# Kernel tuning notes

Hardware: AMD Instinct MI355X
Metric: run time of the kernel (lower is better)

## Reference

```python
import jax, jax.numpy as jnp
import numpy as np

N, C, HW, HEADS = 2048, 16, 8, 4
F = C * HW * HW  # 1024
E = 16384
EPS = 1e-5
NEG_SLOPE = 0.2


def _bn(x, g, b):
    # training-mode BatchNorm2d over (N, H, W)
    m = x.mean(axis=(0, 2, 3), keepdims=True)
    v = x.var(axis=(0, 2, 3), keepdims=True)
    return (x - m) * jax.lax.rsqrt(v + EPS) * g[None, :, None, None] + b[None, :, None, None]


def _conv1x1(x, w, b):
    # 1x1 conv == per-pixel linear: w is [out_c, in_c]
    return jnp.einsum('nchw,oc->nohw', x, w) + b[None, :, None, None]


def _gatv2(xf, edge_index, wl, bl, wr, br, att, bias_gat):
    # xf: [N, F] node features
    xl = (xf @ wl + bl).reshape(N, HEADS, F)  # source-side transform (lin_l)
    xr = (xf @ wr + br).reshape(N, HEADS, F)  # target-side transform (lin_r)
    src, dst = edge_index[0], edge_index[1]
    loops = jnp.arange(N)
    # PyG default: remove existing self loops (mask them) then add self loops
    src_f = jnp.concatenate([src, loops])
    dst_f = jnp.concatenate([dst, loops])
    valid = jnp.concatenate([src != dst, jnp.ones((N,), bool)])
    xj = xl[src_f]                                   # [E+N, HEADS, F] gather
    e = jax.nn.leaky_relu(xj + xr[dst_f], negative_slope=NEG_SLOPE)
    logits = jnp.einsum('ehf,hf->eh', e, att)        # [E+N, HEADS]
    logits = jnp.where(valid[:, None], logits, -jnp.inf)
    mx = jax.lax.stop_gradient(jax.ops.segment_max(logits, dst_f, num_segments=N))
    expv = jnp.where(valid[:, None], jnp.exp(logits - mx[dst_f]), 0.0)
    denom = jax.ops.segment_sum(expv, dst_f, num_segments=N)
    alpha = expv / denom[dst_f]                      # segment softmax over incoming edges
    out = jax.ops.segment_sum(alpha[:, :, None] * xj, dst_f, num_segments=N)  # [N, HEADS, F]
    return out.reshape(N, HEADS * F) + bias_gat


def setup_inputs() -> dict:
    key = jax.random.key(0)
    ks = jax.random.split(key, 8)
    s = 0.02
    return {
        'x': jax.random.normal(ks[0], (N, C, HW, HW), jnp.float32),
        'edge_index': jax.random.randint(ks[1], (2, E), 0, N),
        'w1': jax.random.normal(ks[2], (C, C), jnp.float32) * s,
        'b1': jnp.zeros((C,), jnp.float32),
        'g1': jnp.ones((C,), jnp.float32),
        'be1': jnp.zeros((C,), jnp.float32),
        'wl': jax.random.normal(ks[3], (F, HEADS * F), jnp.float32) * s,
        'bl': jnp.zeros((HEADS * F,), jnp.float32),
        'wr': jax.random.normal(ks[4], (F, HEADS * F), jnp.float32) * s,
        'br': jnp.zeros((HEADS * F,), jnp.float32),
        'att': jax.random.normal(ks[5], (HEADS, F), jnp.float32) * s,
        'bias_gat': jnp.zeros((HEADS * F,), jnp.float32),
        'w2': jax.random.normal(ks[6], (C, HEADS * C), jnp.float32) * s,
        'b2': jnp.zeros((C,), jnp.float32),
        'g2': jnp.ones((C,), jnp.float32),
        'be2': jnp.zeros((C,), jnp.float32),
    }


def reference(x, edge_index, w1, b1, g1, be1, wl, bl, wr, br, att, bias_gat, w2, b2, g2, be2):
    res = x
    y = _bn(_conv1x1(x, w1, b1), g1, be1)            # fc1: Conv2d 1x1 + BN
    yf = y.reshape(N, F)
    g = _gatv2(yf, edge_index, wl, bl, wr, br, att, bias_gat)
    g = g.reshape(N, HEADS * C, HW, HW)
    out = _bn(_conv1x1(g, w2, b2), g2, be2)          # fc2: Conv2d 1x1 + BN
    return out + res                                  # DropPath(0.0) == Identity
```

## Files before the change

kernel.cpp:

```cpp
#include <hip/hip_runtime.h>
#include <stdint.h>

#define N_NODES 2048
#define F_DIM   1024
#define HEADS   4
#define NF      4096
#define ROW     8192
#define E_EDGES 16384
#define MAXE    (E_EDGES + N_NODES)
#define BN_EPS  1e-5f
#define NSLOPE  0.2f

typedef unsigned short ushort_t;
typedef __attribute__((ext_vector_type(8))) short bf16x8;
typedef __attribute__((ext_vector_type(4))) float f32x4;
typedef __attribute__((ext_vector_type(8))) unsigned short us8;

__device__ __forceinline__ float b2f(unsigned short u) {
    union { unsigned int i; float f; } x; x.i = ((unsigned int)u) << 16; return x.f;
}
__device__ __forceinline__ unsigned short f2b(float f) {
    union { float f; unsigned int i; } x; x.f = f;
    unsigned int r = x.i + 0x7fffu + ((x.i >> 16) & 1u);
    return (unsigned short)(r >> 16);
}
__device__ __forceinline__ ushort_t ld_canon(const void* src, size_t i, int f32) {
    return f32 ? f2b(((const float*)src)[i]) : ((const ushort_t*)src)[i];
}
__device__ __forceinline__ float ld_f(const void* src, size_t i, int f32) {
    return f32 ? ((const float*)src)[i] : b2f(((const ushort_t*)src)[i]);
}

__device__ __forceinline__ int sniff_f32_blk(const ushort_t* xu, int* lds_flag) {
    int t = threadIdx.x;
    if (t < 64) {
        unsigned e = (xu[2 * t] >> 7) & 0xFF;
        unsigned long long m = __ballot(e >= 0x90u);
        if (t == 0) *lds_flag = (__popcll(m) >= 3) ? 1 : 0;
    }
    __syncthreads();
    return *lds_flag;
}
__device__ __forceinline__ int sniff_i64_blk(const int* ei_raw, int* lds_flag) {
    int t = threadIdx.x;
    if (t < 64) {
        unsigned long long m = __ballot(ei_raw[2 * t + 1] != 0);
        if (t == 0) *lds_flag = (m == 0ull) ? 1 : 0;
    }
    __syncthreads();
    return *lds_flag;
}

__global__ __launch_bounds__(256) void k_prep(
    const void* __restrict__ wl, const void* __restrict__ wr,
    const int* __restrict__ ei_raw, const ushort_t* __restrict__ xu,
    const void* __restrict__ x, const void* __restrict__ w1, const void* __restrict__ b1,
    ushort_t* __restrict__ wT, int* __restrict__ counts,
    ushort_t* __restrict__ y0b, float* __restrict__ ps, float* __restrict__ pq)
{
    __shared__ ushort_t tl[64][65];
    __shared__ float xs[1024];
    __shared__ float sw[256];
    __shared__ float sb[16];
    __shared__ int sfl;
    int b = blockIdx.x, t = threadIdx.x;
    if (b < 2048) {
        int f32 = sniff_f32_blk(xu, &sfl);
        int z = b >> 10, rem = b & 1023;
        int bx = (rem & 63) * 64, by = (rem >> 6) * 64;
        const void* in = z ? wr : wl;
        ushort_t* outT = wT + (size_t)z * 4194304ull;
        #pragma unroll
        for (int i = 0; i < 16; ++i) {
            int idx = t + i * 256;
            int r = idx >> 6, c = idx & 63;
            tl[r][c] = ld_canon(in, (size_t)(by + r) * 4096 + bx + c, f32);
        }
        __syncthreads();
        #pragma unroll
        for (int i = 0; i < 16; ++i) {
            int idx = t + i * 256;
            int r = idx >> 6, c = idx & 63;
            outT[(size_t)(bx + r) * 1024 + by + c] = tl[c][r];
        }
    } else if (b < 2120) {
        int i64 = sniff_i64_blk(ei_raw, &sfl);
        int idx = (b - 2048) * 256 + t;
        if (idx < E_EDGES) {
            int s = i64 ? ei_raw[2 * idx] : ei_raw[idx];
            int d = i64 ? ei_raw[2 * (E_EDGES + idx)] : ei_raw[E_EDGES + idx];
            if (s != d) atomicAdd(&counts[d], 1);
        } else if (idx < MAXE) {
            atomicAdd(&counts[idx - E_EDGES], 1);
        }
    } else {
        int bid = b - 2120;
        int f32 = sniff_f32_blk(xu, &sfl);
        sw[t] = ld_f(w1, t, f32);
        if (t < 16) sb[t] = ld_f(b1, t, f32);
        int wave = t >> 6, lane = t & 63;
        float s[4] = {0,0,0,0}, q[4] = {0,0,0,0};
        for (int nn = 0; nn < 8; ++nn) {
            int n = bid * 8 + nn;
            __syncthreads();
            #pragma unroll
            for (int i = 0; i < 4; ++i) {
                int idx = t + i * 256;
                xs[idx] = ld_f(x, (size_t)n * 1024 + idx, f32);
            }
            __syncthreads();
            #pragma unroll
            for (int i = 0; i < 4; ++i) {
                int o = wave * 4 + i;
                float acc = sb[o];
                #pragma unroll
                for (int c = 0; c < 16; ++c) acc += xs[c * 64 + lane] * sw[o * 16 + c];
                y0b[(size_t)n * 1024 + o * 64 + lane] = f2b(acc);
                s[i] += acc; q[i] += acc * acc;
            }
        }
        #pragma unroll
        for (int i = 0; i < 4; ++i)
            for (int mm = 1; mm < 64; mm <<= 1) {
                s[i] += __shfl_xor(s[i], mm);
                q[i] += __shfl_xor(q[i], mm);
            }
        if (lane == 0)
            #pragma unroll
            for (int i = 0; i < 4; ++i) {
                ps[bid * 16 + wave * 4 + i] = s[i];
                pq[bid * 16 + wave * 4 + i] = q[i];
            }
    }
}

__global__ __launch_bounds__(256) void k_scatnorm(
    const int* __restrict__ ei_raw, const int* __restrict__ counts,
    int* __restrict__ cursor, int* __restrict__ offs, int* __restrict__ esrc,
    const ushort_t* __restrict__ y0b,
    const float* __restrict__ ps, const float* __restrict__ pq,
    const void* __restrict__ g1, const void* __restrict__ be1,
    const ushort_t* __restrict__ xu, ushort_t* __restrict__ xf)
{
    __shared__ int offl[2048];
    __shared__ int ts[256];
    __shared__ int sfl;
    __shared__ float red[2][64];
    __shared__ float scs[16], shs[16];
    int t = threadIdx.x;
    if (blockIdx.x < 72) {
        int i64 = sniff_i64_blk(ei_raw, &sfl);
        int loc[8]; int tot = 0;
        #pragma unroll
        for (int j = 0; j < 8; ++j) { loc[j] = counts[t * 8 + j]; tot += loc[j]; }
        ts[t] = tot; __syncthreads();
        for (int s = 1; s < 256; s <<= 1) {
            int v = (t >= s) ? ts[t - s] : 0;
            __syncthreads();
            ts[t] += v;
            __syncthreads();
        }
        int run = ts[t] - tot;
        #pragma unroll
        for (int j = 0; j < 8; ++j) { offl[t * 8 + j] = run; run += loc[j]; }
        __syncthreads();
        if (blockIdx.x == 0) {
            #pragma unroll
            for (int j = 0; j < 8; ++j) offs[t * 8 + j] = offl[t * 8 + j];
            if (t == 255) offs[2048] = run;
        }
        int idx = blockIdx.x * 256 + t;
        if (idx < E_EDGES) {
            int s = i64 ? ei_raw[2 * idx] : ei_raw[idx];
            int d = i64 ? ei_raw[2 * (E_EDGES + idx)] : ei_raw[E_EDGES + idx];
            if (s != d) esrc[offl[d] + atomicAdd(&cursor[d], 1)] = s;
        } else if (idx < MAXE) {
            int n = idx - E_EDGES;
            esrc[offl[n] + atomicAdd(&cursor[n], 1)] = n;
        }
    } else {
        int f32 = sniff_f32_blk(xu, &sfl);
        int lane = t & 63, wv = t >> 6;
        float s = 0.f, q = 0.f;
        #pragma unroll
        for (int i = 0; i < 16; ++i) { s += ps[i * 256 + t]; q += pq[i * 256 + t]; }
        s += __shfl_xor(s, 16); q += __shfl_xor(q, 16);
        s += __shfl_xor(s, 32); q += __shfl_xor(q, 32);
        if (lane < 16) { red[0][wv * 16 + lane] = s; red[1][wv * 16 + lane] = q; }
        __syncthreads();
        if (t < 16) {
            float S = red[0][t] + red[0][16 + t] + red[0][32 + t] + red[0][48 + t];
            float Q = red[1][t] + red[1][16 + t] + red[1][32 + t] + red[1][48 + t];
            const float inv = 1.0f / 131072.0f;
            float mean = S * inv;
            float var  = Q * inv - mean * mean;
            float sc = ld_f(g1, t, f32) * rsqrtf(var + BN_EPS);
            scs[t] = sc;
            shs[t] = ld_f(be1, t, f32) - mean * sc;
        }
        __syncthreads();
        size_t base = (size_t)(blockIdx.x - 72) * 4096 + t * 16;
        int ch = ((int)(base >> 6)) & 15;
        float sc = scs[ch], sh = shs[ch];
        us8 v0 = *(const us8*)(y0b + base), v1 = *(const us8*)(y0b + base + 8);
        us8 o0, o1;
        #pragma unroll
        for (int j = 0; j < 8; ++j) {
            o0[j] = f2b(b2f(v0[j]) * sc + sh);
            o1[j] = f2b(b2f(v1[j]) * sc + sh);
        }
        *(us8*)(xf + base) = o0;
        *(us8*)(xf + base + 8) = o1;
    }
}

__global__ __launch_bounds__(512) void k_gemm(
    const ushort_t* __restrict__ A, const ushort_t* __restrict__ BT,
    const void* __restrict__ blr, const void* __restrict__ brr,
    const ushort_t* __restrict__ xu, ushort_t* __restrict__ out)
{
    __shared__ __align__(16) ushort_t smem[65536];
    __shared__ int sfl;
    int f32 = sniff_f32_blk(xu, &sfl);
    int tid = threadIdx.x;
    int wv = tid >> 6, ln = tid & 63;
    int m0 = blockIdx.y * 256, n0 = blockIdx.x * 256;
    int wm = (wv >> 2) * 128, wn = (wv & 3) * 64;
    int lr = ln & 15, quad = ln >> 4;
    int key = (lr >> 1) & 3;

    f32x4 acc[8][4];
    #pragma unroll
    for (int i = 0; i < 8; ++i)
        #pragma unroll
        for (int j = 0; j < 4; ++j) acc[i][j] = (f32x4){0.f, 0.f, 0.f, 0.f};

    auto stage_panel = [&](const ushort_t* G, int row0, int kt, int slot, int which) {
        ushort_t* base = smem + which * 32768 + slot * 8192;
        #pragma unroll
        for (int j = 0; j < 2; ++j) {
            int c = wv * 128 + j * 64 + ln;
            int r = c >> 2;
            int q = (c & 3) ^ ((r >> 1) & 3);
            const ushort_t* g = G + (size_t)(row0 + r) * 1024 + kt * 32 + q * 8;
            __builtin_amdgcn_global_load_lds(
                (const __attribute__((address_space(1))) void*)g,
                (__attribute__((address_space(3))) void*)(base + (wv * 128 + j * 64) * 8),
                16, 0, 0);
        }
    };

    auto compute_tile = [&](int t) {
        const ushort_t* Ab = smem + (t & 3) * 8192;
        const ushort_t* Bb = smem + 32768 + (t & 3) * 8192;
        bf16x8 bfrag[4];
        #pragma unroll
        for (int j = 0; j < 4; ++j) {
            int col = wn + j * 16 + lr;
            bfrag[j] = *(const bf16x8*)(Bb + col * 32 + ((quad ^ key) * 8));
        }
        #pragma unroll
        for (int i = 0; i < 8; ++i) {
            int row = wm + i * 16 + lr;
            bf16x8 af = *(const bf16x8*)(Ab + row * 32 + ((quad ^ key) * 8));
            #pragma unroll
            for (int j = 0; j < 4; ++j)
                acc[i][j] = __builtin_amdgcn_mfma_f32_16x16x32_bf16(af, bfrag[j], acc[i][j], 0, 0, 0);
        }
    };

    stage_panel(A, m0, 0, 0, 0); stage_panel(BT, n0, 0, 0, 1);
    stage_panel(A, m0, 1, 1, 0); stage_panel(BT, n0, 1, 1, 1);
    stage_panel(A, m0, 2, 2, 0); stage_panel(BT, n0, 2, 2, 1);

    #pragma unroll 1
    for (int t = 0; t < 29; ++t) {
        asm volatile("s_waitcnt vmcnt(8)" ::: "memory");
        __builtin_amdgcn_s_barrier();
        int tn = t + 3;
        stage_panel(A, m0, tn, tn & 3, 0);
        stage_panel(BT, n0, tn, tn & 3, 1);
        compute_tile(t);
    }
    asm volatile("s_waitcnt vmcnt(8)" ::: "memory");
    __builtin_amdgcn_s_barrier();
    compute_tile(29);
    asm volatile("s_waitcnt vmcnt(4)" ::: "memory");
    __builtin_amdgcn_s_barrier();
    compute_tile(30);
    asm volatile("s_waitcnt vmcnt(0)" ::: "memory");
    __builtin_amdgcn_s_barrier();
    compute_tile(31);

    __syncthreads();
    float bj[4];
    #pragma unroll
    for (int j = 0; j < 4; ++j) {
        int colg = n0 + wn + j * 16 + lr;
        bj[j] = (colg < 4096) ? ld_f(blr, colg, f32) : ld_f(brr, colg - 4096, f32);
    }
    ushort_t* cs = smem;
    #pragma unroll
    for (int ph = 0; ph < 2; ++ph) {
        if ((wv >> 2) == ph) {
            #pragma unroll
            for (int i = 0; i < 8; ++i)
                #pragma unroll
                for (int j = 0; j < 4; ++j) {
                    int col = wn + j * 16 + lr;
                    #pragma unroll
                    for (int r = 0; r < 4; ++r)
                        cs[(i * 16 + quad * 4 + r) * 264 + col] = f2b(acc[i][j][r] + bj[j]);
                }
        }
        __syncthreads();
        #pragma unroll
        for (int rr = 0; rr < 8; ++rr) {
            int slot = rr * 512 + tid;
            int row = slot >> 5, seg = slot & 31;
            us8 v = *(const us8*)&cs[row * 264 + seg * 8];
            *(us8*)(out + (size_t)(m0 + ph * 128 + row) * ROW + n0 + seg * 8) = v;
        }
        __syncthreads();
    }
}

__global__ __launch_bounds__(64) void k_gat(
    const ushort_t* __restrict__ xlr,
    const void* __restrict__ att, const void* __restrict__ bg,
    const ushort_t* __restrict__ xu,
    const int* __restrict__ offsets, const int* __restrict__ esrc,
    ushort_t* __restrict__ g)
{
    int bx = blockIdx.x;
    int d = bx >> 2, h = bx & 3;
    int l = threadIdx.x;
    int f32;
    {
        unsigned e = (xu[2 * l] >> 7) & 0xFF;
        unsigned long long m = __ballot(e >= 0x90u);
        f32 = (__popcll(m) >= 3) ? 1 : 0;
    }
    int off = offsets[d], deg = offsets[d + 1] - off;
    size_t hF = (size_t)h * F_DIM + l * 16;

    float xrv[16], attv[16];
    {
        const ushort_t* xp = xlr + ((size_t)d * ROW + NF + hF);
        us8 x0 = *(const us8*)xp, x1 = *(const us8*)(xp + 8);
        #pragma unroll
        for (int j = 0; j < 8; ++j) {
            xrv[j] = b2f(x0[j]); xrv[8 + j] = b2f(x1[j]);
            attv[j]     = ld_f(att, hF + j, f32);
            attv[8 + j] = ld_f(att, hF + 8 + j, f32);
        }
    }
    float acc[16];
    #pragma unroll
    for (int j = 0; j < 16; ++j) acc[j] = 0.f;
    float s_run = 0.f;

    for (int c0 = 0; c0 < deg; c0 += 64) {
        int cnt = min(64, deg - c0);
        int eidx = esrc[off + c0 + (l < cnt ? l : 0)];
        int e = 0;
        for (; e + 3 < cnt; e += 4) {
            int i0 = __shfl(eidx, e),     i1 = __shfl(eidx, e + 1);
            int i2 = __shfl(eidx, e + 2), i3 = __shfl(eidx, e + 3);
            const ushort_t* p0 = xlr + ((size_t)i0 * ROW + hF);
            const ushort_t* p1 = xlr + ((size_t)i1 * ROW + hF);
            const ushort_t* p2 = xlr + ((size_t)i2 * ROW + hF);
            const ushort_t* p3 = xlr + ((size_t)i3 * ROW + hF);
            us8 v0[4], v1[4];
            v0[0] = *(const us8*)p0; v1[0] = *(const us8*)(p0 + 8);
            v0[1] = *(const us8*)p1; v1[1] = *(const us8*)(p1 + 8);
            v0[2] = *(const us8*)p2; v1[2] = *(const us8*)(p2 + 8);
            v0[3] = *(const us8*)p3; v1[3] = *(const us8*)(p3 + 8);
            float tt[4];
            #pragma unroll
            for (int k = 0; k < 4; ++k) {
                float t0 = 0.f;
                #pragma unroll
                for (int j = 0; j < 8; ++j) {
                    float u;
                    u = b2f(v0[k][j]) + xrv[j];     u = u > 0.f ? u : NSLOPE * u; t0 += u * attv[j];
                    u = b2f(v1[k][j]) + xrv[8 + j]; u = u > 0.f ? u : NSLOPE * u; t0 += u * attv[8 + j];
                }
                tt[k] = t0;
            }
            #pragma unroll
            for (int mm = 1; mm < 64; mm <<= 1) {
                tt[0] += __shfl_xor(tt[0], mm);
                tt[1] += __shfl_xor(tt[1], mm);
                tt[2] += __shfl_xor(tt[2], mm);
                tt[3] += __shfl_xor(tt[3], mm);
            }
            float w0 = __expf(tt[0]), w1 = __expf(tt[1]);
            float w2v = __expf(tt[2]), w3 = __expf(tt[3]);
            s_run += w0 + w1 + w2v + w3;
            #pragma unroll
            for (int j = 0; j < 8; ++j) {
                acc[j]     += w0 * b2f(v0[0][j]) + w1 * b2f(v0[1][j])
                            + w2v * b2f(v0[2][j]) + w3 * b2f(v0[3][j]);
                acc[8 + j] += w0 * b2f(v1[0][j]) + w1 * b2f(v1[1][j])
                            + w2v * b2f(v1[2][j]) + w3 * b2f(v1[3][j]);
            }
        }
        for (; e < cnt; ++e) {
            int i0 = __shfl(eidx, e);
            const ushort_t* p = xlr + ((size_t)i0 * ROW + hF);
            us8 a0 = *(const us8*)p, a1 = *(const us8*)(p + 8);
            float t0 = 0.f;
            #pragma unroll
            for (int j = 0; j < 8; ++j) {
                float u;
                u = b2f(a0[j]) + xrv[j];     u = u > 0.f ? u : NSLOPE * u; t0 += u * attv[j];
                u = b2f(a1[j]) + xrv[8 + j]; u = u > 0.f ? u : NSLOPE * u; t0 += u * attv[8 + j];
            }
            #pragma unroll
            for (int mm = 1; mm < 64; mm <<= 1) t0 += __shfl_xor(t0, mm);
            float w0 = __expf(t0);
            s_run += w0;
            #pragma unroll
            for (int j = 0; j < 8; ++j) {
                acc[j]     += w0 * b2f(a0[j]);
                acc[8 + j] += w0 * b2f(a1[j]);
            }
        }
    }
    float inv = 1.0f / s_run;
    ushort_t* gp = g + ((size_t)d * NF + hF);
    us8 outv0, outv1;
    #pragma unroll
    for (int j = 0; j < 8; ++j) {
        outv0[j] = f2b(acc[j] * inv + ld_f(bg, hF + j, f32));
        outv1[j] = f2b(acc[8 + j] * inv + ld_f(bg, hF + 8 + j, f32));
    }
    *(us8*)gp = outv0;
    *(us8*)(gp + 8) = outv1;
}

__global__ __launch_bounds__(256) void k_fc2(
    const ushort_t* __restrict__ g, const void* __restrict__ w2, const void* __restrict__ b2,
    const ushort_t* __restrict__ xu,
    ushort_t* __restrict__ zb, float* __restrict__ ps, float* __restrict__ pq)
{
    __shared__ float gs[4096];
    __shared__ float sw[1024];
    __shared__ float sb[16];
    __shared__ int sfl;
    int f32 = sniff_f32_blk(xu, &sfl);
    int tid = threadIdx.x;
    #pragma unroll
    for (int i = 0; i < 4; ++i) sw[tid + i * 256] = ld_f(w2, tid + i * 256, f32);
    if (tid < 16) sb[tid] = ld_f(b2, tid, f32);
    int wave = tid >> 6, lane = tid & 63;
    float s[4] = {0,0,0,0}, q[4] = {0,0,0,0};
    for (int nn = 0; nn < 2; ++nn) {
        int n = blockIdx.x * 2 + nn;
        __syncthreads();
        {
            const ushort_t* gp = g + (size_t)n * 4096 + tid * 16;
            us8 v0 = *(const us8*)gp, v1 = *(const us8*)(gp + 8);
            #pragma unroll
            for (int j = 0; j < 8; ++j) {
                gs[tid * 16 + j] = b2f(v0[j]);
                gs[tid * 16 + 8 + j] = b2f(v1[j]);
            }
        }
        __syncthreads();
        float acc[4];
        #pragma unroll
        for (int i = 0; i < 4; ++i) acc[i] = sb[wave * 4 + i];
        #pragma unroll 8
        for (int k = 0; k < 64; ++k) {
            float gv = gs[k * 64 + lane];
            #pragma unroll
            for (int i = 0; i < 4; ++i)
                acc[i] += gv * sw[(wave * 4 + i) * 64 + k];
        }
        #pragma unroll
        for (int i = 0; i < 4; ++i) {
            zb[(size_t)n * 1024 + (wave * 4 + i) * 64 + lane] = f2b(acc[i]);
            s[i] += acc[i]; q[i] += acc[i] * acc[i];
        }
    }
    #pragma unroll
    for (int i = 0; i < 4; ++i)
        for (int mm = 1; mm < 64; mm <<= 1) {
            s[i] += __shfl_xor(s[i], mm);
            q[i] += __shfl_xor(q[i], mm);
        }
    if (lane == 0)
        #pragma unroll
        for (int i = 0; i < 4; ++i) {
            ps[blockIdx.x * 16 + wave * 4 + i] = s[i];
            pq[blockIdx.x * 16 + wave * 4 + i] = q[i];
        }
}

__global__ __launch_bounds__(256) void k_out(
    const ushort_t* __restrict__ zb, const void* __restrict__ x,
    const float* __restrict__ ps, const float* __restrict__ pq,
    const void* __restrict__ g2, const void* __restrict__ be2,
    void* __restrict__ out)
{
    __shared__ float red[2][64];
    __shared__ float scs[16], shs[16];
    __shared__ int sfl;
    int f32 = sniff_f32_blk((const ushort_t*)x, &sfl);
    int t = threadIdx.x, lane = t & 63, wv = t >> 6;
    float s = 0.f, q = 0.f;
    #pragma unroll
    for (int i = 0; i < 64; ++i) { s += ps[i * 256 + t]; q += pq[i * 256 + t]; }
    s += __shfl_xor(s, 16); q += __shfl_xor(q, 16);
    s += __shfl_xor(s, 32); q += __shfl_xor(q, 32);
    if (lane < 16) { red[0][wv * 16 + lane] = s; red[1][wv * 16 + lane] = q; }
    __syncthreads();
    if (t < 16) {
        float S = red[0][t] + red[0][16 + t] + red[0][32 + t] + red[0][48 + t];
        float Q = red[1][t] + red[1][16 + t] + red[1][32 + t] + red[1][48 + t];
        const float inv = 1.0f / 131072.0f;
        float mean = S * inv;
        float var  = Q * inv - mean * mean;
        float sc = ld_f(g2, t, f32) * rsqrtf(var + BN_EPS);
        scs[t] = sc;
        shs[t] = ld_f(be2, t, f32) - mean * sc;
    }
    __syncthreads();
    size_t base = (size_t)blockIdx.x * 4096;
    #pragma unroll
    for (int i = 0; i < 16; ++i) {
        size_t k = base + t + i * 256;
        int ch = ((int)k >> 6) & 15;
        float val = b2f(zb[k]) * scs[ch] + shs[ch] + ld_f(x, k, f32);
        if (f32) ((float*)out)[k] = val;
        else     ((ushort_t*)out)[k] = f2b(val);
    }
}

extern "C" void kernel_launch(void* const* d_in, const int* in_sizes, int n_in,
                              void* d_out, int out_size, void* d_ws, size_t ws_size,
                              hipStream_t stream)
{
    const void* x   = d_in[0];
    const void* ei  = d_in[1];
    const void* w1  = d_in[2];
    const void* b1  = d_in[3];
    const void* g1  = d_in[4];
    const void* be1 = d_in[5];
    const void* wl  = d_in[6];
    const void* bl  = d_in[7];
    const void* wr  = d_in[8];
    const void* br  = d_in[9];
    const void* att = d_in[10];
    const void* bg  = d_in[11];
    const void* w2  = d_in[12];
    const void* b2  = d_in[13];
    const void* g2  = d_in[14];
    const void* be2 = d_in[15];
    (void)in_sizes; (void)n_in; (void)out_size; (void)ws_size;

    char* wsb = (char*)d_ws;
    size_t o = 0;
    auto alloc = [&](size_t bytes) -> void* {
        void* p = wsb + o;
        o = (o + bytes + 255) & ~(size_t)255;
        return p;
    };
    ushort_t* y0b   = (ushort_t*)alloc(2097152ull * 2);
    ushort_t* xf    = (ushort_t*)alloc(2097152ull * 2);
    ushort_t* zb    = (ushort_t*)alloc(2097152ull * 2);
    ushort_t* wT    = (ushort_t*)alloc(8388608ull * 2);
    ushort_t* gbuf  = wT;
    ushort_t* xlr   = (ushort_t*)alloc(16777216ull * 2);
    float* p1s = (float*)alloc(256 * 16 * 4);
    float* p1q = (float*)alloc(256 * 16 * 4);
    float* p2s = (float*)alloc(1024 * 16 * 4);
    float* p2q = (float*)alloc(1024 * 16 * 4);
    int* counts = (int*)alloc(2048 * 4);
    int* cursor = (int*)alloc(2048 * 4);
    int* offs   = (int*)alloc(2049 * 4);
    int* esrc   = (int*)alloc(MAXE * 4);

    hipMemsetAsync(counts, 0, 2 * 2048 * 4, stream);
    k_prep<<<2376, 256, 0, stream>>>(wl, wr, (const int*)ei, (const ushort_t*)x,
                                     x, w1, b1, wT, counts, y0b, p1s, p1q);
    k_scatnorm<<<584, 256, 0, stream>>>((const int*)ei, counts, cursor, offs, esrc,
                                        y0b, p1s, p1q, g1, be1, (const ushort_t*)x, xf);
    k_gemm<<<dim3(32, 8), 512, 0, stream>>>(xf, wT, bl, br, (const ushort_t*)x, xlr);
    k_gat<<<N_NODES * HEADS, 64, 0, stream>>>(xlr, att, bg, (const ushort_t*)x, offs, esrc, gbuf);
    k_fc2<<<1024, 256, 0, stream>>>(gbuf, w2, b2, (const ushort_t*)x, zb, p2s, p2q);
    k_out<<<512, 256, 0, stream>>>(zb, x, p2s, p2q, g2, be2, d_out);
}
```

Baseline: 261.7 us.

## Vectorize weight transpose and reshape GEMM pipeline to depth two with occupancy hint

The weight transpose in k_prep now loads and stores 8 bf16 values per access, with a padded LDS tile, instead of scalar element accesses. The GEMM prefetch depth drops from three tiles in flight to two, inside a single uniform loop with a sched_barrier. It also requests two blocks per CU through launch_bounds. Together these aim to cut transpose memory traffic and register pressure, trading some latency hiding for possible occupancy gains, though 128 KB of LDS per block may stop two blocks from fitting anyway.

```diff
diff --git a/kernel.cpp b/kernel.cpp
--- a/kernel.cpp
+++ b/kernel.cpp
@@ -58,7 +58,7 @@
     ushort_t* __restrict__ wT, int* __restrict__ counts,
     ushort_t* __restrict__ y0b, float* __restrict__ ps, float* __restrict__ pq)
 {
-    __shared__ ushort_t tl[64][65];
+    __shared__ ushort_t tl[64][72];
     __shared__ float xs[1024];
     __shared__ float sw[256];
     __shared__ float sb[16];
@@ -71,17 +71,31 @@
         const void* in = z ? wr : wl;
         ushort_t* outT = wT + (size_t)z * 4194304ull;
         #pragma unroll
-        for (int i = 0; i < 16; ++i) {
+        for (int i = 0; i < 2; ++i) {
             int idx = t + i * 256;
-            int r = idx >> 6, c = idx & 63;
-            tl[r][c] = ld_canon(in, (size_t)(by + r) * 4096 + bx + c, f32);
-        }
-        __syncthreads();
-        #pragma unroll
-        for (int i = 0; i < 16; ++i) {
+            int r = idx >> 3, c8 = (idx & 7) * 8;
+            size_t gi = (size_t)(by + r) * 4096 + bx + c8;
+            us8 v;
+            if (f32) {
+                const float* fp = (const float*)in + gi;
+                float4 a = *(const float4*)fp;
+                float4 bb = *(const float4*)(fp + 4);
+                v[0] = f2b(a.x); v[1] = f2b(a.y); v[2] = f2b(a.z); v[3] = f2b(a.w);
+                v[4] = f2b(bb.x); v[5] = f2b(bb.y); v[6] = f2b(bb.z); v[7] = f2b(bb.w);
+            } else {
+                v = *(const us8*)((const ushort_t*)in + gi);
+            }
+            *(us8*)(&tl[r][c8]) = v;
+        }
+        __syncthreads();
+        #pragma unroll
+        for (int i = 0; i < 2; ++i) {
             int idx = t + i * 256;
-            int r = idx >> 6, c = idx & 63;
-            outT[(size_t)(bx + r) * 1024 + by + c] = tl[c][r];
+            int rr = idx >> 3, cc8 = (idx & 7) * 8;
+            us8 v;
+            #pragma unroll
+            for (int j = 0; j < 8; ++j) v[j] = tl[cc8 + j][rr];
+            *(us8*)(outT + (size_t)(bx + rr) * 1024 + by + cc8) = v;
         }
     } else if (b < 2120) {
         int i64 = sniff_i64_blk(ei_raw, &sfl);
@@ -214,7 +228,7 @@
     }
 }
 
-__global__ __launch_bounds__(512) void k_gemm(
+__global__ __launch_bounds__(512, 2) void k_gemm(
     const ushort_t* __restrict__ A, const ushort_t* __restrict__ BT,
     const void* __restrict__ blr, const void* __restrict__ brr,
     const ushort_t* __restrict__ xu, ushort_t* __restrict__ out)
@@ -227,7 +241,7 @@
     int m0 = blockIdx.y * 256, n0 = blockIdx.x * 256;
     int wm = (wv >> 2) * 128, wn = (wv & 3) * 64;
     int lr = ln & 15, quad = ln >> 4;
-    int key = (lr >> 1) & 3;
+    int swz8 = (quad ^ ((lr >> 1) & 3)) * 8;
 
     f32x4 acc[8][4];
     #pragma unroll
@@ -235,64 +249,54 @@
         #pragma unroll
         for (int j = 0; j < 4; ++j) acc[i][j] = (f32x4){0.f, 0.f, 0.f, 0.f};
 
-    auto stage_panel = [&](const ushort_t* G, int row0, int kt, int slot, int which) {
-        ushort_t* base = smem + which * 32768 + slot * 8192;
+    auto stage = [&](int tt) {
+        int slot = tt & 3;
         #pragma unroll
         for (int j = 0; j < 2; ++j) {
-            int c = wv * 128 + j * 64 + ln;
-            int r = c >> 2;
-            int q = (c & 3) ^ ((r >> 1) & 3);
-            const ushort_t* g = G + (size_t)(row0 + r) * 1024 + kt * 32 + q * 8;
+            int cbase = j * 512 + wv * 64;
+            int ci = cbase + ln;
+            int r = ci >> 2, psg = ci & 3;
+            int lsg = psg ^ ((r >> 1) & 3);
+            const ushort_t* ga = A + (size_t)(m0 + r) * 1024 + tt * 32 + lsg * 8;
             __builtin_amdgcn_global_load_lds(
-                (const __attribute__((address_space(1))) void*)g,
-                (__attribute__((address_space(3))) void*)(base + (wv * 128 + j * 64) * 8),
-                16, 0, 0);
+                (const __attribute__((address_space(1))) void*)ga,
+                (__attribute__((address_space(3))) void*)(&smem[slot * 8192 + cbase * 8]), 16, 0, 0);
+            const ushort_t* gb = BT + (size_t)(n0 + r) * 1024 + tt * 32 + lsg * 8;
+            __builtin_amdgcn_global_load_lds(
+                (const __attribute__((address_space(1))) void*)gb,
+                (__attribute__((address_space(3))) void*)(&smem[32768 + slot * 8192 + cbase * 8]), 16, 0, 0);
         }
     };
 
-    auto compute_tile = [&](int t) {
-        const ushort_t* Ab = smem + (t & 3) * 8192;
-        const ushort_t* Bb = smem + 32768 + (t & 3) * 8192;
-        bf16x8 bfrag[4];
-        #pragma unroll
-        for (int j = 0; j < 4; ++j) {
-            int col = wn + j * 16 + lr;
-            bfrag[j] = *(const bf16x8*)(Bb + col * 32 + ((quad ^ key) * 8));
-        }
+    auto compute = [&](int tt) {
+        int slot = tt & 3;
+        const ushort_t* Ab = smem + slot * 8192;
+        const ushort_t* Bb = smem + 32768 + slot * 8192;
+        bf16x8 bfr[4];
+        #pragma unroll
+        for (int j = 0; j < 4; ++j)
+            bfr[j] = *(const bf16x8*)(&Bb[(wn + j * 16 + lr) * 32 + swz8]);
         #pragma unroll
         for (int i = 0; i < 8; ++i) {
-            int row = wm + i * 16 + lr;
-            bf16x8 af = *(const bf16x8*)(Ab + row * 32 + ((quad ^ key) * 8));
+            bf16x8 af = *(const bf16x8*)(&Ab[(wm + i * 16 + lr) * 32 + swz8]);
             #pragma unroll
             for (int j = 0; j < 4; ++j)
-                acc[i][j] = __builtin_amdgcn_mfma_f32_16x16x32_bf16(af, bfrag[j], acc[i][j], 0, 0, 0);
+                acc[i][j] = __builtin_amdgcn_mfma_f32_16x16x32_bf16(af, bfr[j], acc[i][j], 0, 0, 0);
         }
     };
 
-    stage_panel(A, m0, 0, 0, 0); stage_panel(BT, n0, 0, 0, 1);
-    stage_panel(A, m0, 1, 1, 0); stage_panel(BT, n0, 1, 1, 1);
-    stage_panel(A, m0, 2, 2, 0); stage_panel(BT, n0, 2, 2, 1);
-
+    stage(0); stage(1);
     #pragma unroll 1
-    for (int t = 0; t < 29; ++t) {
-        asm volatile("s_waitcnt vmcnt(8)" ::: "memory");
+    for (int t = 0; t < 32; ++t) {
+        if (t < 31) asm volatile("s_waitcnt vmcnt(4)" ::: "memory");
+        else        asm volatile("s_waitcnt vmcnt(0)" ::: "memory");
         __builtin_amdgcn_s_barrier();
-        int tn = t + 3;
-        stage_panel(A, m0, tn, tn & 3, 0);
-        stage_panel(BT, n0, tn, tn & 3, 1);
-        compute_tile(t);
-    }
-    asm volatile("s_waitcnt vmcnt(8)" ::: "memory");
-    __builtin_amdgcn_s_barrier();
-    compute_tile(29);
-    asm volatile("s_waitcnt vmcnt(4)" ::: "memory");
-    __builtin_amdgcn_s_barrier();
-    compute_tile(30);
-    asm volatile("s_waitcnt vmcnt(0)" ::: "memory");
-    __builtin_amdgcn_s_barrier();
-    compute_tile(31);
-
+        __builtin_amdgcn_sched_barrier(0);
+        if (t < 30) stage(t + 2);
+        compute(t);
+    }
     __syncthreads();
+
     float bj[4];
     #pragma unroll
     for (int j = 0; j < 4; ++j) {
```

Result: faster. 254.7 us (-2.7%).
